# Kernel tuning notes

Measured on AMD Instinct MI355X. Metric: run time of the kernel, lower is better.

The kernel has to match this reference:

```python
import jax, jax.numpy as jnp
import numpy as np

B, S, IN_DIM = 4, 2048, 768
D, M, K, H = 24, 8192, 32, 256
Q = 8
SCALES = 4
TWO_PI = 2.0 * np.pi


def _ln(x, g, b):
    m = jnp.mean(x, -1, keepdims=True)
    v = jnp.mean((x - m) ** 2, -1, keepdims=True)
    return (x - m) * jax.lax.rsqrt(v + 1e-5) * g + b


def setup_inputs() -> dict:
    key = jax.random.key(0)
    ks = jax.random.split(key, 12)
    def n(k, shape, s=0.02):
        return (jax.random.normal(k, shape) * s).astype(jnp.float32)
    f32 = jnp.float32
    return dict(
        x=jax.random.normal(ks[0], (B, S, IN_DIM), dtype=f32),
        W_in=n(ks[1], (3 * D, IN_DIM)), b_in=jnp.zeros((3 * D,), f32),
        ln_in_g=jnp.ones((3 * D,), f32), ln_in_b=jnp.zeros((3 * D,), f32),
        ricci=jnp.eye(D, dtype=f32),
        fractal_w=jnp.ones((SCALES,), f32),
        keys=jax.random.normal(ks[2], (M, D), dtype=f32),
        key_phase_W=n(ks[3], (H, IN_DIM)), key_phase_b=jnp.zeros((H,), f32),
        entangle_key=n(ks[4], (H,), 0.1),
        holo_re=n(ks[5], (M, H), 0.1), holo_im=n(ks[6], (M, H), 0.1),
        readout_W=n(ks[7], (3 * D, 2 * H)), readout_b=jnp.zeros((3 * D,), f32),
        W_out=n(ks[8], (IN_DIM, 3 * D)), b_out=jnp.zeros((IN_DIM,), f32),
        ln_out_g=jnp.ones((IN_DIM,), f32), ln_out_b=jnp.zeros((IN_DIM,), f32),
        quantum_phase=jax.random.normal(ks[9], (M, Q), dtype=f32),
    )


def reference(x, W_in, b_in, ln_in_g, ln_in_b, ricci, fractal_w, keys,
              key_phase_W, key_phase_b, entangle_key, holo_re, holo_im,
              readout_W, readout_b, W_out, b_out, ln_out_g, ln_out_b,
              quantum_phase):
    # encode_to_manifold: Linear -> LN -> GELU -> view (B,S,D,3) -> ricci einsum
    z = jax.nn.gelu(_ln(x @ W_in.T + b_in, ln_in_g, ln_in_b), approximate=False)
    z = z.reshape(B, S, D, 3)
    z = jnp.einsum('bseq,ed->bsdq', z, ricci)
    q = z.mean(axis=3)  # (B,S,D)

    # fractal cdist: cdist(q/2^s, k/2^s) = cdist(q,k)/2^s -> single pass * factor
    d2 = (jnp.sum(q * q, -1)[..., None]
          + jnp.sum(keys * keys, -1)[None, None, :]
          - 2.0 * jnp.einsum('bsd,md->bsm', q, keys))
    d = jnp.sqrt(jnp.maximum(d2, 0.0))  # (B,S,M)
    fw = jax.nn.softmax(fractal_w)
    scale = jnp.sum(fw / (2.0 ** jnp.arange(SCALES, dtype=jnp.float32)))
    dist = d * scale  # temperature buffer == 1.0

    # top-K smallest distances
    neg_top, itop = jax.lax.top_k(-dist, K)  # (B,S,K)
    w = jax.nn.softmax(neg_top, axis=-1)     # softmax(-dtop)

    # holographic read: unbind with conj(key) from gathered holograms
    phase = TWO_PI * jax.nn.sigmoid(x @ key_phase_W.T + key_phase_b)  # (B,S,H)
    Kf = jnp.fft.fft(jnp.exp(1j * phase), axis=-1) * jnp.exp(1j * entangle_key)
    Hol = holo_re + 1j * holo_im  # (M,H) complex
    # weighted sum over slots first, then multiply conj(Kf) (same math, cheaper)
    Hmix = jnp.einsum('bsk,bskh->bsh', w.astype(Hol.dtype), Hol[itop])
    vhat = jnp.fft.ifft(jnp.conj(Kf) * Hmix, axis=-1)
    feat = jnp.concatenate([vhat.real, vhat.imag], axis=-1)  # (B,S,2H)

    triplet = feat @ readout_W.T + readout_b
    out = jax.nn.gelu(_ln(triplet @ W_out.T + b_out, ln_out_g, ln_out_b),
                      approximate=False)

    # quantum gain (any_fire = False for this configuration)
    phases = jnp.tanh(quantum_phase[itop]).mean(-1)  # (B,S,K)
    gain = 1.0 + 0.02 * jnp.sum(w * phases, -1, keepdims=True)
    return out * gain
```

## Files before the change

kernel.cpp:

```cpp
#include <hip/hip_runtime.h>
#include <hip/hip_bf16.h>
#include <math.h>

#define NROWS 8192
#define INDIM 768
#define TD    72
#define DM    24
#define MKEYS 8192
#define KSEL  32
#define HN    256
#define K3CAND 128

#define TWO_PI_F 6.283185307179586f

typedef __attribute__((ext_vector_type(8))) short short8_t;
typedef __attribute__((ext_vector_type(4))) float f32x4;

__device__ __forceinline__ float gelu_exact(float v){
  return 0.5f * v * (1.0f + erff(v * 0.7071067811865476f));
}

__device__ __forceinline__ unsigned short bf16rn(float f){
  unsigned u = __float_as_uint(f);
  unsigned r = u + 0x7FFFu + ((u >> 16) & 1u);
  return (unsigned short)(r >> 16);
}

__device__ __forceinline__ float rowmin16(float v){
  int s, p;
  s = __float_as_int(v); p = __builtin_amdgcn_update_dpp(s, s, 0x111, 0xF, 0xF, false);
  v = fminf(v, __int_as_float(p));
  s = __float_as_int(v); p = __builtin_amdgcn_update_dpp(s, s, 0x112, 0xF, 0xF, false);
  v = fminf(v, __int_as_float(p));
  s = __float_as_int(v); p = __builtin_amdgcn_update_dpp(s, s, 0x114, 0xF, 0xF, false);
  v = fminf(v, __int_as_float(p));
  s = __float_as_int(v); p = __builtin_amdgcn_update_dpp(s, s, 0x118, 0xF, 0xF, false);
  v = fminf(v, __int_as_float(p));
  return v;
}

__global__ __launch_bounds__(256) void k0_gprep(
    const float* __restrict__ RW, float* __restrict__ Grp, float* __restrict__ Gip)
{
  __shared__ float sre[16][260];
  __shared__ float sim_[16][260];
  __shared__ float twc[HN], tws[HN];
  const int t = threadIdx.x;
  const int o0 = blockIdx.x * 16;
  {
    const float a = (float)t * (TWO_PI_F / 256.f);
    twc[t] = cosf(a); tws[t] = sinf(a);
  }
  const int r = t >> 4, cg = t & 15;
  const int o = o0 + r;
#pragma unroll
  for (int j = 0; j < 16; j++) {
    const int n = cg + 16 * j;
    const int hb = __brev((unsigned)n) >> 24;
    float cr = 0.f, ci = 0.f;
    if (o < TD) { cr = RW[(size_t)o * 512 + n]; ci = RW[(size_t)o * 512 + 256 + n]; }
    sre[r][hb] = cr; sim_[r][hb] = ci;
  }
  __syncthreads();
  const int t16 = t & 15;
  for (int s = 0; s < 8; s++) {
    const int half = 1 << s;
#pragma unroll
    for (int p = 0; p < 8; p++) {
      const int bi = t16 + 16 * p;
      const int jj = bi & (half - 1);
      const int base = (bi >> s) << (s + 1);
      const int i0 = base + jj, i1 = i0 + half;
      const int tw = jj << (7 - s);
      const float wr = twc[tw], wi = -tws[tw];
      const float ar = sre[r][i0], ai = sim_[r][i0];
      const float br = sre[r][i1], b2 = sim_[r][i1];
      const float tr = wr * br - wi * b2, ti = wr * b2 + wi * br;
      sre[r][i0] = ar + tr; sim_[r][i0] = ai + ti;
      sre[r][i1] = ar - tr; sim_[r][i1] = ai - ti;
    }
    __syncthreads();
  }
#pragma unroll
  for (int p = 0; p < 16; p++) {
    const int h = t16 + 16 * p;
    const size_t base = ((size_t)(h >> 2) * 128 + o) * 4 + (h & 3);
    Grp[base] = sre[r][h];
    Gip[base] = sim_[r][h];
  }
}

__global__ __launch_bounds__(256) void kw_split(
    const float* __restrict__ Wp, unsigned short* __restrict__ Wphi,
    unsigned short* __restrict__ Wplo)
{
  const int i4 = blockIdx.x * 256 + threadIdx.x;
  const float4 v = ((const float4*)Wp)[i4];
  float vv[4] = {v.x, v.y, v.z, v.w};
  ushort4 hh, ll;
  unsigned short* hp = (unsigned short*)&hh;
  unsigned short* lp = (unsigned short*)&ll;
#pragma unroll
  for (int j = 0; j < 4; j++) {
    const unsigned short h = bf16rn(vv[j]);
    const float hf = __uint_as_float(((unsigned)h) << 16);
    hp[j] = h; lp[j] = bf16rn(vv[j] - hf);
  }
  ((ushort4*)Wphi)[i4] = hh;
  ((ushort4*)Wplo)[i4] = ll;
}

__global__ __launch_bounds__(256) void kwo_split(
    const float* __restrict__ Wo, unsigned short* __restrict__ Wohi,
    unsigned short* __restrict__ Wolo)
{
  const int idx = blockIdx.x * 256 + threadIdx.x;
  const int row = idx / 96, k = idx % 96;
  const float v = (k < TD) ? Wo[(size_t)row * TD + k] : 0.f;
  const unsigned short h = bf16rn(v);
  const float hf = __uint_as_float(((unsigned)h) << 16);
  Wohi[idx] = h;
  Wolo[idx] = bf16rn(v - hf);
}

__global__ __launch_bounds__(256) void k1_encode(
    const float* __restrict__ x, const float* __restrict__ Wi,
    const float* __restrict__ bi, const float* __restrict__ gi,
    const float* __restrict__ bbi, const float* __restrict__ ricci,
    float* __restrict__ qvec, float* __restrict__ qnorm)
{
  __shared__ float xs[16][132];
  __shared__ float Ws[TD][132];
  __shared__ float zs[16][73];
  __shared__ float zb[16][25];
  const int t = threadIdx.x;
  const int r2 = t >> 4, ks = (t >> 3) & 1, u = t & 7;
  const int row0 = blockIdx.x * 16;

  float acc[9];
#pragma unroll
  for (int j = 0; j < 9; j++) acc[j] = 0.f;

  for (int kc = 0; kc < 6; kc++) {
    __syncthreads();
#pragma unroll
    for (int i = 0; i < 2; i++) {
      int idx = t + 256 * i;
      int rr = idx >> 5, kk = (idx & 31) << 2;
      *(float4*)&xs[rr][kk] = *(const float4*)&x[(size_t)(row0 + rr) * INDIM + kc * 128 + kk];
    }
#pragma unroll
    for (int i = 0; i < 9; i++) {
      int idx = t + 256 * i;
      int rr = idx >> 5, kk = (idx & 31) << 2;
      *(float4*)&Ws[rr][kk] = *(const float4*)&Wi[(size_t)rr * INDIM + kc * 128 + kk];
    }
    __syncthreads();
    const int kb = ks * 64;
#pragma unroll 4
    for (int kq = 0; kq < 16; kq++) {
      const float4 xv = *(const float4*)&xs[r2][kb + kq * 4];
#pragma unroll
      for (int j = 0; j < 9; j++) {
        const float4 wv = *(const float4*)&Ws[u + 8 * j][kb + kq * 4];
        acc[j] = fmaf(xv.x, wv.x, fmaf(xv.y, wv.y, fmaf(xv.z, wv.z, fmaf(xv.w, wv.w, acc[j]))));
      }
    }
  }
#pragma unroll
  for (int j = 0; j < 9; j++) acc[j] += __shfl_xor(acc[j], 8);

  float yv[9];
  float ps = 0.f, pq = 0.f;
#pragma unroll
  for (int j = 0; j < 9; j++) {
    const int o = u + 8 * j;
    yv[j] = acc[j] + bi[o];
    ps += yv[j]; pq += yv[j] * yv[j];
  }
#pragma unroll
  for (int m = 1; m < 8; m <<= 1) { ps += __shfl_xor(ps, m); pq += __shfl_xor(pq, m); }
  const float mean = ps * (1.f / 72.f);
  const float var  = pq * (1.f / 72.f) - mean * mean;
  const float rstd = rsqrtf(var + 1e-5f);
#pragma unroll
  for (int j = 0; j < 9; j++) {
    const int o = u + 8 * j;
    const float z = gelu_exact((yv[j] - mean) * rstd * gi[o] + bbi[o]);
    if (ks == 0) zs[r2][o] = z;
  }
  __syncthreads();
  {
    const int kt = t & 15;
    for (int e = kt; e < 24; e += 16)
      zb[r2][e] = (zs[r2][3 * e] + zs[r2][3 * e + 1] + zs[r2][3 * e + 2]) * (1.f / 3.f);
  }
  __syncthreads();
  {
    const int kt = t & 15;
    float qnp = 0.f;
    for (int d = kt; d < 24; d += 16) {
      float qd = 0.f;
#pragma unroll
      for (int e = 0; e < 24; e++) qd = fmaf(zb[r2][e], ricci[e * 24 + d], qd);
      qvec[(size_t)(row0 + r2) * DM + d] = qd;
      qnp = fmaf(qd, qd, qnp);
    }
#pragma unroll
    for (int m = 1; m < 16; m <<= 1) qnp += __shfl_xor(qnp, m, 16);
    if (kt == 0) qnorm[row0 + r2] = qnp;
  }
}

__global__ __launch_bounds__(256) void k2_prep(
    const float* __restrict__ keys, const float* __restrict__ qp,
    float* __restrict__ kn, float* __restrict__ pm,
    unsigned short* __restrict__ khi, unsigned short* __restrict__ klo,
    float* __restrict__ kmx)
{
  __shared__ float red[256];
  const int t = threadIdx.x;
  const int m = blockIdx.x * 256 + t;
  float kv[24];
#pragma unroll
  for (int d = 0; d < DM; d += 4) {
    const float4 v = *(const float4*)&keys[(size_t)m * DM + d];
    kv[d] = v.x; kv[d + 1] = v.y; kv[d + 2] = v.z; kv[d + 3] = v.w;
  }
  float s = 0.f;
#pragma unroll
  for (int d = 0; d < DM; d++) s = fmaf(kv[d], kv[d], s);
  kn[m] = s;
  float p = 0.f;
#pragma unroll
  for (int q = 0; q < 8; q++) p += tanhf(qp[(size_t)m * 8 + q]);
  pm[m] = p * 0.125f;
#pragma unroll
  for (int d = 0; d < DM; d++) {
    const unsigned short h = bf16rn(kv[d]);
    const float hf = __uint_as_float(((unsigned)h) << 16);
    const unsigned short l = bf16rn(kv[d] - hf);
    khi[(size_t)m * 32 + d] = h;
    klo[(size_t)m * 32 + d] = l;
  }
#pragma unroll
  for (int d = DM; d < 32; d++) { khi[(size_t)m * 32 + d] = 0; klo[(size_t)m * 32 + d] = 0; }
  red[t] = s;
  __syncthreads();
  for (int off = 128; off > 0; off >>= 1) {
    if (t < off) red[t] = fmaxf(red[t], red[t + off]);
    __syncthreads();
  }
  if (t == 0) kmx[blockIdx.x] = red[0];
}

__global__ __launch_bounds__(1024, 4) void k3_topk(
    const float* __restrict__ qvec, const float* __restrict__ qnorm,
    const float* __restrict__ keys, const float* __restrict__ kn,
    const unsigned short* __restrict__ khi, const unsigned short* __restrict__ klo,
    const float* __restrict__ kmx,
    const float* __restrict__ fw,  const float* __restrict__ pm,
    float* __restrict__ w_out, int* __restrict__ itop_out, float* __restrict__ gain_out)
{
  __shared__ float qsm[32][25];
  __shared__ float qns[32];
  __shared__ unsigned short qh_l[32][32];
  __shared__ unsigned short ql_l[32][32];
  __shared__ float gmins[64][33];
  __shared__ float Ts[32];
  __shared__ float Tm2s[32];
  __shared__ unsigned glive[2];
  __shared__ int cnt[32];
  __shared__ int      candI[32][K3CAND];
  __shared__ unsigned candV[32][K3CAND];
  __shared__ float wV[32][KSEL];
  __shared__ int   wI[32][KSEL];
  __shared__ float knmax_s;

  const int t = threadIdx.x;
  const int w = t >> 6, lane = t & 63;
  const int colid = lane & 15;
  const int kgrp  = lane >> 4;
  const int row0 = blockIdx.x * 32;

  if (t < 32 * DM) qsm[t / DM][t % DM] = qvec[(size_t)row0 * DM + t];
  if (t < 32) { qns[t] = qnorm[row0 + t]; cnt[t] = 0; }
  if (t < 2) glive[t] = 0u;
  if (t == 0) { float m = 0.f; for (int i = 0; i < 32; i++) m = fmaxf(m, kmx[i]); knmax_s = m; }
  __syncthreads();
  {
    const int r = t >> 5, k = t & 31;
    const float v = (k < DM) ? qsm[r][k] : 0.f;
    const unsigned short h = bf16rn(v);
    const float hf = __uint_as_float(((unsigned)h) << 16);
    qh_l[r][k] = h;
    ql_l[r][k] = bf16rn(v - hf);
  }
  __syncthreads();

  const short8_t ah0 = *(const short8_t*)&qh_l[colid][kgrp * 8];
  const short8_t al0 = *(const short8_t*)&ql_l[colid][kgrp * 8];
  const short8_t ah1 = *(const short8_t*)&qh_l[16 + colid][kgrp * 8];
  const short8_t al1 = *(const short8_t*)&ql_l[16 + colid][kgrp * 8];
  float qn8[8];
#pragma unroll
  for (int reg = 0; reg < 4; reg++) {
    qn8[reg]     = qns[kgrp * 4 + reg];
    qn8[reg + 4] = qns[16 + kgrp * 4 + reg];
  }

  for (int u = 0; u < 4; u++) {
    const int g = w + 16 * u;
    const int nbase = g * 128;
    float mn[8];
#pragma unroll
    for (int j = 0; j < 8; j++) {
      const int key = nbase + j * 16 + colid;
      const short8_t bh = *(const short8_t*)&khi[(size_t)key * 32 + kgrp * 8];
      const short8_t bl = *(const short8_t*)&klo[(size_t)key * 32 + kgrp * 8];
      const float knv = kn[key];
      f32x4 c0 = {0.f, 0.f, 0.f, 0.f}, c1 = {0.f, 0.f, 0.f, 0.f};
      c0 = __builtin_amdgcn_mfma_f32_16x16x32_bf16(ah0, bh, c0, 0, 0, 0);
      c1 = __builtin_amdgcn_mfma_f32_16x16x32_bf16(ah1, bh, c1, 0, 0, 0);
      c0 = __builtin_amdgcn_mfma_f32_16x16x32_bf16(ah0, bl, c0, 0, 0, 0);
      c1 = __builtin_amdgcn_mfma_f32_16x16x32_bf16(ah1, bl, c1, 0, 0, 0);
      c0 = __builtin_amdgcn_mfma_f32_16x16x32_bf16(al0, bh, c0, 0, 0, 0);
      c1 = __builtin_amdgcn_mfma_f32_16x16x32_bf16(al1, bh, c1, 0, 0, 0);
#pragma unroll
      for (int reg = 0; reg < 4; reg++) {
        const float d0 = fmaf(-2.f, c0[reg], qn8[reg] + knv);
        const float d1 = fmaf(-2.f, c1[reg], qn8[reg + 4] + knv);
        if (j == 0) { mn[reg] = d0; mn[reg + 4] = d1; }
        else        { mn[reg] = fminf(mn[reg], d0); mn[reg + 4] = fminf(mn[reg + 4], d1); }
      }
    }
#pragma unroll
    for (int reg = 0; reg < 4; reg++) {
      const float v0 = rowmin16(mn[reg]);
      const float v1 = rowmin16(mn[reg + 4]);
      if (colid == 15) {
        gmins[g][kgrp * 4 + reg] = v0;
        gmins[g][16 + kgrp * 4 + reg] = v1;
      }
    }
  }
  __syncthreads();

  {
    const int r = t & 31, i = t >> 5;
    const float v0 = gmins[i * 2][r], v1 = gmins[i * 2 + 1][r];
    int rk0 = 0, eq0 = 0, rk1 = 0, eq1 = 0;
    for (int g = 0; g < 64; g++) {
      const float gv = gmins[g][r];
      rk0 += (gv < v0); eq0 += (gv == v0);
      rk1 += (gv < v1); eq1 += (gv == v1);
    }
    if (rk0 <= 31 && rk0 + eq0 > 31) Ts[r] = v0;
    if (rk1 <= 31 && rk1 + eq1 > 31) Ts[r] = v1;
  }
  __syncthreads();
  if (t < 32) {
    const float T = Ts[t];
    const float mu = 2e-4f * sqrtf(fmaxf(qns[t], 0.f) * knmax_s) + 1e-6f;
    Tm2s[t] = T + fabsf(T) * 1e-6f + 2.f * mu;
  }
  __syncthreads();
  {
    const int r = t & 31, i = t >> 5;
    const unsigned b0 = (gmins[i * 2][r]     <= Tm2s[r]) ? 1u : 0u;
    const unsigned b1 = (gmins[i * 2 + 1][r] <= Tm2s[r]) ? 2u : 0u;
    const unsigned bits = (b0 | b1) << ((i * 2) & 31);
    if (bits) atomicOr(&glive[i >> 4], bits);
  }
  __syncthreads();

  float tm8[8];
#pragma unroll
  for (int reg = 0; reg < 4; reg++) {
    tm8[reg]     = Tm2s[kgrp * 4 + reg];
    tm8[reg + 4] = Tm2s[16 + kgrp * 4 + reg];
  }

  for (int u = 0; u < 4; u++) {
    const int g = w + 16 * u;
    if (!((glive[g >> 5] >> (g & 31)) & 1u)) continue;
    const int nbase = g * 128;
#pragma unroll
    for (int j = 0; j < 8; j++) {
      const int key = nbase + j * 16 + colid;
      const short8_t bh = *(const short8_t*)&khi[(size_t)key * 32 + kgrp * 8];
      const short8_t bl = *(const short8_t*)&klo[(size_t)key * 32 + kgrp * 8];
      const float knv = kn[key];
      f32x4 c0 = {0.f, 0.f, 0.f, 0.f}, c1 = {0.f, 0.f, 0.f, 0.f};
      c0 = __builtin_amdgcn_mfma_f32_16x16x32_bf16(ah0, bh, c0, 0, 0, 0);
      c1 = __builtin_amdgcn_mfma_f32_16x16x32_bf16(ah1, bh, c1, 0, 0, 0);
      c0 = __builtin_amdgcn_mfma_f32_16x16x32_bf16(ah0, bl, c0, 0, 0, 0);
      c1 = __builtin_amdgcn_mfma_f32_16x16x32_bf16(ah1, bl, c1, 0, 0, 0);
      c0 = __builtin_amdgcn_mfma_f32_16x16x32_bf16(al0, bh, c0, 0, 0, 0);
      c1 = __builtin_amdgcn_mfma_f32_16x16x32_bf16(al1, bh, c1, 0, 0, 0);
#pragma unroll
      for (int reg = 0; reg < 4; reg++) {
        const float d0 = fmaf(-2.f, c0[reg], qn8[reg] + knv);
        if (d0 <= tm8[reg]) {
          const int row = kgrp * 4 + reg;
          const int pos = atomicAdd(&cnt[row], 1);
          if (pos < K3CAND) candI[row][pos] = key;
        }
        const float d1 = fmaf(-2.f, c1[reg], qn8[reg + 4] + knv);
        if (d1 <= tm8[reg + 4]) {
          const int row = 16 + kgrp * 4 + reg;
          const int pos = atomicAdd(&cnt[row], 1);
          if (pos < K3CAND) candI[row][pos] = key;
        }
      }
    }
  }
  for (int idx = t; idx < 32 * KSEL; idx += 1024) { wV[idx >> 5][idx & 31] = 1e30f; wI[idx >> 5][idx & 31] = 0; }
  __syncthreads();

  {
    const int r = t >> 5, kt = t & 31;
    const int C = min(cnt[r], K3CAND);
    const float qnr = qns[r];
    for (int ci = kt; ci < C; ci += 32) {
      const int key = candI[r][ci];
      float kv[24];
#pragma unroll
      for (int d = 0; d < DM; d += 4) {
        const float4 v = *(const float4*)&keys[(size_t)key * DM + d];
        kv[d] = v.x; kv[d + 1] = v.y; kv[d + 2] = v.z; kv[d + 3] = v.w;
      }
      float dot = 0.f;
#pragma unroll
      for (int d = 0; d < DM; d++) dot = fmaf(kv[d], qsm[r][d], dot);
      const float d2 = fmaf(-2.f, dot, qnr + kn[key]);
      candV[r][ci] = __float_as_uint(fmaxf(d2, 0.f));
    }
  }
  __syncthreads();

  {
    const int r = t >> 5, kt = t & 31;
    const int C = min(cnt[r], K3CAND);
    for (int ci = kt; ci < C; ci += 32) {
      const unsigned v = candV[r][ci];
      const unsigned key = (unsigned)candI[r][ci];
      int rk = 0;
      for (int j = 0; j < C; j++) {
        const unsigned vj = candV[r][j];
        rk += (vj < v) || (vj == v && (unsigned)candI[r][j] < key);
      }
      if (rk < KSEL) { wV[r][rk] = __uint_as_float(v); wI[r][rk] = (int)key; }
    }
  }
  __syncthreads();

  float sc;
  {
    const float f0 = fw[0], f1 = fw[1], f2 = fw[2], f3 = fw[3];
    const float mx = fmaxf(fmaxf(f0, f1), fmaxf(f2, f3));
    const float e0 = expf(f0 - mx), e1 = expf(f1 - mx), e2 = expf(f2 - mx), e3 = expf(f3 - mx);
    sc = (e0 + 0.5f * e1 + 0.25f * e2 + 0.125f * e3) / (e0 + e1 + e2 + e3);
  }
  if (t < 512) {
    const int r = t >> 4, kt = t & 15;
    const float dA = sqrtf(wV[r][kt]) * sc;
    const float dB = sqrtf(wV[r][kt + 16]) * sc;
    float mn = fminf(dA, dB);
#pragma unroll
    for (int m = 1; m < 16; m <<= 1) mn = fminf(mn, __shfl_xor(mn, m, 16));
    const float eA = expf(mn - dA), eB = expf(mn - dB);
    float s = eA + eB;
#pragma unroll
    for (int m = 1; m < 16; m <<= 1) s += __shfl_xor(s, m, 16);
    const float w0 = eA / s, w1 = eB / s;
    const int k0 = wI[r][kt], k1 = wI[r][kt + 16];
    float gp = w0 * pm[k0] + w1 * pm[k1];
#pragma unroll
    for (int m = 1; m < 16; m <<= 1) gp += __shfl_xor(gp, m, 16);
    const size_t row = (size_t)(row0 + r);
    w_out[row * KSEL + kt] = w0;      w_out[row * KSEL + kt + 16] = w1;
    itop_out[row * KSEL + kt] = k0;   itop_out[row * KSEL + kt + 16] = k1;
    if (kt == 0) gain_out[row] = 1.f + 0.02f * gp;
  }
}

__global__ __launch_bounds__(512) void k4a_pgemm(
    const float* __restrict__ x, const unsigned short* __restrict__ Wphi,
    const unsigned short* __restrict__ Wplo, const float* __restrict__ bp,
    float* __restrict__ p)
{
  const int t = threadIdx.x;
  const int w = t >> 6, lane = t & 63;
  const int colid = lane & 15, kgrp = lane >> 4;
  const int wm = w >> 2, wn = w & 3;
  const int row0 = blockIdx.x * 32;
  const int arow = row0 + wm * 16 + colid;

  f32x4 acc0 = {0.f, 0.f, 0.f, 0.f};
  f32x4 acc1 = {0.f, 0.f, 0.f, 0.f};
  f32x4 acc2 = {0.f, 0.f, 0.f, 0.f};
  f32x4 acc3 = {0.f, 0.f, 0.f, 0.f};

  for (int kc = 0; kc < 24; kc++) {
    const int kb = kc * 32 + kgrp * 8;
    float xv[8];
    *(float4*)&xv[0] = *(const float4*)&x[(size_t)arow * INDIM + kb];
    *(float4*)&xv[4] = *(const float4*)&x[(size_t)arow * INDIM + kb + 4];
    short8_t ah, al;
#pragma unroll
    for (int i = 0; i < 8; i++) {
      const unsigned short h = bf16rn(xv[i]);
      const float hf = __uint_as_float(((unsigned)h) << 16);
      ah[i] = (short)h;
      al[i] = (short)bf16rn(xv[i] - hf);
    }
#pragma unroll
    for (int ct = 0; ct < 4; ct++) {
      const int col = wn * 64 + ct * 16 + colid;
      const short8_t bh = *(const short8_t*)&Wphi[(size_t)col * INDIM + kb];
      const short8_t bl = *(const short8_t*)&Wplo[(size_t)col * INDIM + kb];
      f32x4* pa = (ct == 0) ? &acc0 : (ct == 1) ? &acc1 : (ct == 2) ? &acc2 : &acc3;
      *pa = __builtin_amdgcn_mfma_f32_16x16x32_bf16(ah, bh, *pa, 0, 0, 0);
      *pa = __builtin_amdgcn_mfma_f32_16x16x32_bf16(al, bh, *pa, 0, 0, 0);
      *pa = __builtin_amdgcn_mfma_f32_16x16x32_bf16(ah, bl, *pa, 0, 0, 0);
    }
  }
#pragma unroll
  for (int ct = 0; ct < 4; ct++) {
    const int col = wn * 64 + ct * 16 + colid;
    const float b = bp[col];
    const f32x4 a = (ct == 0) ? acc0 : (ct == 1) ? acc1 : (ct == 2) ? acc2 : acc3;
#pragma unroll
    for (int reg = 0; reg < 4; reg++) {
      const int row = row0 + wm * 16 + kgrp * 4 + reg;
      p[(size_t)row * HN + col] = a[reg] + b;
    }
  }
}

__global__ __launch_bounds__(256) void k4b_fft(
    const float* __restrict__ p, const float* __restrict__ ek,
    float* __restrict__ kf_re, float* __restrict__ kf_im)
{
  __shared__ float2 c[16][273];
  __shared__ float twc[HN], tws[HN];
  const int t = threadIdx.x;
  const int row0 = blockIdx.x * 16;
  {
    const float a = (float)t * (TWO_PI_F / 256.f);
    twc[t] = cosf(a); tws[t] = sinf(a);
  }
  {
    const int hb = __brev((unsigned)t) >> 24;
    const int hbi = hb + (hb >> 5);
#pragma unroll
    for (int i = 0; i < 16; i++) {
      const float pv = p[(size_t)(row0 + i) * HN + t];
      const float sg = 1.f / (1.f + expf(-pv));
      float sn, cs;
      __sincosf(TWO_PI_F * sg, &sn, &cs);
      c[i][hbi] = make_float2(cs, sn);
    }
  }
  __syncthreads();
  const int r = t >> 4, t16 = t & 15;
  for (int s = 0; s < 8; s++) {
    const int half = 1 << s;
#pragma unroll
    for (int pp = 0; pp < 8; pp++) {
      const int bi = t16 + 16 * pp;
      const int jj = bi & (half - 1);
      const int base = (bi >> s) << (s + 1);
      const int i0 = base + jj, i1 = i0 + half;
      const int tw = jj << (7 - s);
      const float wr = twc[tw], wi = -tws[tw];
      const int p0 = i0 + (i0 >> 5), p1 = i1 + (i1 >> 5);
      const float2 A = c[r][p0];
      const float2 B = c[r][p1];
      const float tr = wr * B.x - wi * B.y, ti = wr * B.y + wi * B.x;
      c[r][p0] = make_float2(A.x + tr, A.y + ti);
      c[r][p1] = make_float2(A.x - tr, A.y - ti);
    }
    __syncthreads();
  }
  {
    float esn, ecs;
    __sincosf(ek[t], &esn, &ecs);
    const int ti = t + (t >> 5);
#pragma unroll
    for (int i = 0; i < 16; i++) {
      const float2 v = c[i][ti];
      const size_t o = (size_t)(row0 + i) * HN + t;
      kf_re[o] = v.x * ecs - v.y * esn;
      kf_im[o] = v.x * esn + v.y * ecs;
    }
  }
}

__global__ __launch_bounds__(256) void k5_holo(
    const float* __restrict__ holo_re, const float* __restrict__ holo_im,
    const float* __restrict__ kf_re, const float* __restrict__ kf_im,
    const float* __restrict__ w_ws, const int* __restrict__ itop_ws,
    const float* __restrict__ Grp, const float* __restrict__ Gip,
    const float* __restrict__ rb, float* __restrict__ triplet)
{
  __shared__ __align__(16) float ysr[8][260];
  __shared__ __align__(16) float ysi[8][260];
  __shared__ float red[4][8][128];
  __shared__ float wsm[8][KSEL];
  __shared__ int   ism[8][KSEL];
  const int t = threadIdx.x;
  const int w = t >> 6, lane = t & 63;
  const int row0 = blockIdx.x * 8;

  {
    const int rr = t >> 5, k2 = t & 31;
    wsm[rr][k2] = w_ws[(size_t)(row0 + rr) * KSEL + k2];
    ism[rr][k2] = itop_ws[(size_t)(row0 + rr) * KSEL + k2];
  }
  __syncthreads();

#pragma unroll
  for (int pass = 0; pass < 2; pass++) {
    const int row = w + 4 * pass;
    float4 hr4 = {0.f, 0.f, 0.f, 0.f};
    float4 hi4 = {0.f, 0.f, 0.f, 0.f};
#pragma unroll 8
    for (int k2 = 0; k2 < KSEL; k2++) {
      const int m = ism[row][k2];
      const float wk = wsm[row][k2];
      const float4 re4 = *(const float4*)&holo_re[(size_t)m * HN + lane * 4];
      const float4 im4 = *(const float4*)&holo_im[(size_t)m * HN + lane * 4];
      hr4.x = fmaf(wk, re4.x, hr4.x); hr4.y = fmaf(wk, re4.y, hr4.y);
      hr4.z = fmaf(wk, re4.z, hr4.z); hr4.w = fmaf(wk, re4.w, hr4.w);
      hi4.x = fmaf(wk, im4.x, hi4.x); hi4.y = fmaf(wk, im4.y, hi4.y);
      hi4.z = fmaf(wk, im4.z, hi4.z); hi4.w = fmaf(wk, im4.w, hi4.w);
    }
    const size_t o = (size_t)(row0 + row) * HN + lane * 4;
    const float4 kr4 = *(const float4*)&kf_re[o];
    const float4 ki4 = *(const float4*)&kf_im[o];
    float4 yr4, yi4;
    yr4.x = kr4.x * hr4.x + ki4.x * hi4.x;  yi4.x = kr4.x * hi4.x - ki4.x * hr4.x;
    yr4.y = kr4.y * hr4.y + ki4.y * hi4.y;  yi4.y = kr4.y * hi4.y - ki4.y * hr4.y;
    yr4.z = kr4.z * hr4.z + ki4.z * hi4.z;  yi4.z = kr4.z * hi4.z - ki4.z * hr4.z;
    yr4.w = kr4.w * hr4.w + ki4.w * hi4.w;  yi4.w = kr4.w * hi4.w - ki4.w * hr4.w;
    *(float4*)&ysr[row][lane * 4] = yr4;
    *(float4*)&ysi[row][lane * 4] = yi4;
  }
  __syncthreads();

  float acc[8][2];
#pragma unroll
  for (int rr = 0; rr < 8; rr++) { acc[rr][0] = 0.f; acc[rr][1] = 0.f; }
#pragma unroll 4
  for (int i = 0; i < 16; i++) {
    const int h4 = w * 16 + i;
    const float4 gra = *(const float4*)&Grp[((size_t)h4 * 128 + lane) * 4];
    const float4 gia = *(const float4*)&Gip[((size_t)h4 * 128 + lane) * 4];
    const float4 grb = *(const float4*)&Grp[((size_t)h4 * 128 + 64 + lane) * 4];
    const float4 gib = *(const float4*)&Gip[((size_t)h4 * 128 + 64 + lane) * 4];
#pragma unroll
    for (int rr = 0; rr < 8; rr++) {
      const float4 yr4 = *(const float4*)&ysr[rr][h4 * 4];
      const float4 yi4 = *(const float4*)&ysi[rr][h4 * 4];
      acc[rr][0] = fmaf(yr4.x, gra.x, fmaf(yr4.y, gra.y, fmaf(yr4.z, gra.z, fmaf(yr4.w, gra.w, acc[rr][0]))));
      acc[rr][0] = fmaf(yi4.x, gia.x, fmaf(yi4.y, gia.y, fmaf(yi4.z, gia.z, fmaf(yi4.w, gia.w, acc[rr][0]))));
      acc[rr][1] = fmaf(yr4.x, grb.x, fmaf(yr4.y, grb.y, fmaf(yr4.z, grb.z, fmaf(yr4.w, grb.w, acc[rr][1]))));
      acc[rr][1] = fmaf(yi4.x, gib.x, fmaf(yi4.y, gib.y, fmaf(yi4.z, gib.z, fmaf(yi4.w, gib.w, acc[rr][1]))));
    }
  }
#pragma unroll
  for (int rr = 0; rr < 8; rr++) {
    red[w][rr][lane] = acc[rr][0];
    red[w][rr][64 + lane] = acc[rr][1];
  }
  __syncthreads();

  for (int idx = t; idx < 8 * 128; idx += 256) {
    const int rr = idx >> 7, o = idx & 127;
    if (o < TD) {
      const float s = red[0][rr][o] + red[1][rr][o] + red[2][rr][o] + red[3][rr][o];
      triplet[(size_t)(row0 + rr) * TD + o] = rb[o] + s * (1.f / 256.f);
    }
  }
}

__global__ __launch_bounds__(256) void k6_mfma(
    const float* __restrict__ triplet, const unsigned short* __restrict__ Wohi,
    const unsigned short* __restrict__ Wolo, const float* __restrict__ bo,
    const float* __restrict__ go, const float* __restrict__ bbo,
    const float* __restrict__ gain, float* __restrict__ out)
{
  __shared__ float ys[16][772];
  const int t = threadIdx.x;
  const int w = t >> 6, lane = t & 63;
  const int colid = lane & 15, kgrp = lane >> 4;
  const int row0 = blockIdx.x * 16;
  const int arow = row0 + colid;

  f32x4 acc[12];
#pragma unroll
  for (int ct = 0; ct < 12; ct++) acc[ct] = (f32x4){0.f, 0.f, 0.f, 0.f};

#pragma unroll
  for (int kc = 0; kc < 3; kc++) {
    const int kb = kc * 32 + kgrp * 8;
    float xv[8];
    if (kb < TD) {
      *(float4*)&xv[0] = *(const float4*)&triplet[(size_t)arow * TD + kb];
      *(float4*)&xv[4] = *(const float4*)&triplet[(size_t)arow * TD + kb + 4];
    } else {
#pragma unroll
      for (int i = 0; i < 8; i++) xv[i] = 0.f;
    }
    short8_t ah, al;
#pragma unroll
    for (int i = 0; i < 8; i++) {
      const unsigned short h = bf16rn(xv[i]);
      const float hf = __uint_as_float(((unsigned)h) << 16);
      ah[i] = (short)h; al[i] = (short)bf16rn(xv[i] - hf);
    }
#pragma unroll
    for (int ct = 0; ct < 12; ct++) {
      const int col = w * 192 + ct * 16 + colid;
      const short8_t bh = *(const short8_t*)&Wohi[(size_t)col * 96 + kb];
      const short8_t bl = *(const short8_t*)&Wolo[(size_t)col * 96 + kb];
      acc[ct] = __builtin_amdgcn_mfma_f32_16x16x32_bf16(ah, bh, acc[ct], 0, 0, 0);
      acc[ct] = __builtin_amdgcn_mfma_f32_16x16x32_bf16(al, bh, acc[ct], 0, 0, 0);
      acc[ct] = __builtin_amdgcn_mfma_f32_16x16x32_bf16(ah, bl, acc[ct], 0, 0, 0);
    }
  }
#pragma unroll
  for (int ct = 0; ct < 12; ct++) {
    const int col = w * 192 + ct * 16 + colid;
    const float b = bo[col];
#pragma unroll
    for (int reg = 0; reg < 4; reg++)
      ys[kgrp * 4 + reg][col] = acc[ct][reg] + b;
  }
  __syncthreads();

  const int r = t >> 4, kt = t & 15;
  float s = 0.f, sq = 0.f;
  for (int u = 0; u < 48; u++) {
    const float v = ys[r][kt + 16 * u];
    s += v; sq = fmaf(v, v, sq);
  }
#pragma unroll
  for (int m = 1; m < 16; m <<= 1) { s += __shfl_xor(s, m, 16); sq += __shfl_xor(sq, m, 16); }
  const float mean = s * (1.f / 768.f);
  const float var  = sq * (1.f / 768.f) - mean * mean;
  const float rstd = rsqrtf(var + 1e-5f);
  const float gn = gain[row0 + r];
  for (int u = 0; u < 48; u++) {
    const int e = kt + 16 * u;
    const float v = (ys[r][e] - mean) * rstd * go[e] + bbo[e];
    out[(size_t)(row0 + r) * INDIM + e] = gelu_exact(v) * gn;
  }
}

extern "C" void kernel_launch(void* const* d_in, const int* in_sizes, int n_in,
                              void* d_out, int out_size, void* d_ws, size_t ws_size,
                              hipStream_t stream)
{
  (void)in_sizes; (void)n_in; (void)out_size; (void)ws_size;
  const float* x     = (const float*)d_in[0];
  const float* Wi    = (const float*)d_in[1];
  const float* bi    = (const float*)d_in[2];
  const float* gi    = (const float*)d_in[3];
  const float* bbi   = (const float*)d_in[4];
  const float* ricci = (const float*)d_in[5];
  const float* fw    = (const float*)d_in[6];
  const float* keys  = (const float*)d_in[7];
  const float* Wp    = (const float*)d_in[8];
  const float* bp    = (const float*)d_in[9];
  const float* ek    = (const float*)d_in[10];
  const float* hre   = (const float*)d_in[11];
  const float* him   = (const float*)d_in[12];
  const float* RW    = (const float*)d_in[13];
  const float* rb    = (const float*)d_in[14];
  const float* Wo    = (const float*)d_in[15];
  const float* bo    = (const float*)d_in[16];
  const float* go    = (const float*)d_in[17];
  const float* bbo   = (const float*)d_in[18];
  const float* qp    = (const float*)d_in[19];
  float* out = (float*)d_out;

  char* ws = (char*)d_ws;
  float* qvec    = (float*)(ws + 0);
  float* qnorm   = (float*)(ws + 786432);
  float* kn      = (float*)(ws + 819200);
  float* pm      = (float*)(ws + 851968);
  float* gain    = (float*)(ws + 884736);
  float* w_ws    = (float*)(ws + 917504);
  int*   itop    = (int*)  (ws + 1966080);
  float* triplet = (float*)(ws + 3014656);
  float* kf_re   = (float*)(ws + 5373952);
  float* kf_im   = (float*)(ws + 13762560);
  unsigned short* khi = (unsigned short*)(ws + 22151168);
  unsigned short* klo = (unsigned short*)(ws + 22675456);
  float* kmx     = (float*)(ws + 23199744);
  float* Grp     = (float*)(ws + 23200768);
  float* Gip     = (float*)(ws + 23331840);
  unsigned short* Wphi = (unsigned short*)(ws + 23462912);
  unsigned short* Wplo = (unsigned short*)(ws + 23856128);
  float* pbuf    = (float*)(ws + 24249344);
  unsigned short* Wohi = (unsigned short*)(ws + 32637952);
  unsigned short* Wolo = (unsigned short*)(ws + 32785408);

  k0_gprep<<<dim3(8), dim3(256), 0, stream>>>(RW, Grp, Gip);
  kw_split<<<dim3(192), dim3(256), 0, stream>>>(Wp, Wphi, Wplo);
  kwo_split<<<dim3(288), dim3(256), 0, stream>>>(Wo, Wohi, Wolo);
  k2_prep<<<dim3(MKEYS / 256), dim3(256), 0, stream>>>(keys, qp, kn, pm, khi, klo, kmx);
  k1_encode<<<dim3(NROWS / 16), dim3(256), 0, stream>>>(x, Wi, bi, gi, bbi, ricci, qvec, qnorm);
  k4a_pgemm<<<dim3(NROWS / 32), dim3(512), 0, stream>>>(x, Wphi, Wplo, bp, pbuf);
  k4b_fft<<<dim3(NROWS / 16), dim3(256), 0, stream>>>(pbuf, ek, kf_re, kf_im);
  k3_topk<<<dim3(NROWS / 32), dim3(1024), 0, stream>>>(qvec, qnorm, keys, kn, khi, klo, kmx, fw, pm, w_ws, itop, gain);
  k5_holo<<<dim3(NROWS / 8), dim3(256), 0, stream>>>(hre, him, kf_re, kf_im, w_ws, itop, Grp, Gip, rb, triplet);
  k6_mfma<<<dim3(NROWS / 16), dim3(256), 0, stream>>>(triplet, Wohi, Wolo, bo, go, bbo, gain, out);
}
```

Before: 267.7 us.

## Halve rows per top-k block to 16 and double grid size

Result: slower. 302.2 us (+12.9%).

```diff
diff --git a/kernel.cpp b/kernel.cpp
--- a/kernel.cpp
+++ b/kernel.cpp
@@ -254,7 +254,7 @@
   if (t == 0) kmx[blockIdx.x] = red[0];
 }
 
-__global__ __launch_bounds__(1024, 4) void k3_topk(
+__global__ __launch_bounds__(1024, 8) void k3_topk(
     const float* __restrict__ qvec, const float* __restrict__ qnorm,
     const float* __restrict__ keys, const float* __restrict__ kn,
     const unsigned short* __restrict__ khi, const unsigned short* __restrict__ klo,
@@ -262,33 +262,33 @@
     const float* __restrict__ fw,  const float* __restrict__ pm,
     float* __restrict__ w_out, int* __restrict__ itop_out, float* __restrict__ gain_out)
 {
-  __shared__ float qsm[32][25];
-  __shared__ float qns[32];
-  __shared__ unsigned short qh_l[32][32];
-  __shared__ unsigned short ql_l[32][32];
-  __shared__ float gmins[64][33];
-  __shared__ float Ts[32];
-  __shared__ float Tm2s[32];
+  __shared__ float qsm[16][25];
+  __shared__ float qns[16];
+  __shared__ unsigned short qh_l[16][32];
+  __shared__ unsigned short ql_l[16][32];
+  __shared__ float gmins[64][17];
+  __shared__ float Ts[16];
+  __shared__ float Tm2s[16];
   __shared__ unsigned glive[2];
-  __shared__ int cnt[32];
-  __shared__ int      candI[32][K3CAND];
-  __shared__ unsigned candV[32][K3CAND];
-  __shared__ float wV[32][KSEL];
-  __shared__ int   wI[32][KSEL];
+  __shared__ int cnt[16];
+  __shared__ int      candI[16][K3CAND];
+  __shared__ unsigned candV[16][K3CAND];
+  __shared__ float wV[16][KSEL];
+  __shared__ int   wI[16][KSEL];
   __shared__ float knmax_s;
 
   const int t = threadIdx.x;
   const int w = t >> 6, lane = t & 63;
   const int colid = lane & 15;
   const int kgrp  = lane >> 4;
-  const int row0 = blockIdx.x * 32;
-
-  if (t < 32 * DM) qsm[t / DM][t % DM] = qvec[(size_t)row0 * DM + t];
-  if (t < 32) { qns[t] = qnorm[row0 + t]; cnt[t] = 0; }
+  const int row0 = blockIdx.x * 16;
+
+  if (t < 16 * DM) qsm[t / DM][t % DM] = qvec[(size_t)row0 * DM + t];
+  if (t < 16) { qns[t] = qnorm[row0 + t]; cnt[t] = 0; }
   if (t < 2) glive[t] = 0u;
   if (t == 0) { float m = 0.f; for (int i = 0; i < 32; i++) m = fmaxf(m, kmx[i]); knmax_s = m; }
   __syncthreads();
-  {
+  if (t < 512) {
     const int r = t >> 5, k = t & 31;
     const float v = (k < DM) ? qsm[r][k] : 0.f;
     const unsigned short h = bf16rn(v);
@@ -300,86 +300,65 @@
 
   const short8_t ah0 = *(const short8_t*)&qh_l[colid][kgrp * 8];
   const short8_t al0 = *(const short8_t*)&ql_l[colid][kgrp * 8];
-  const short8_t ah1 = *(const short8_t*)&qh_l[16 + colid][kgrp * 8];
-  const short8_t al1 = *(const short8_t*)&ql_l[16 + colid][kgrp * 8];
-  float qn8[8];
-#pragma unroll
-  for (int reg = 0; reg < 4; reg++) {
-    qn8[reg]     = qns[kgrp * 4 + reg];
-    qn8[reg + 4] = qns[16 + kgrp * 4 + reg];
-  }
+  float qn4[4];
+#pragma unroll
+  for (int reg = 0; reg < 4; reg++) qn4[reg] = qns[kgrp * 4 + reg];
 
   for (int u = 0; u < 4; u++) {
     const int g = w + 16 * u;
     const int nbase = g * 128;
-    float mn[8];
+    float mn[4];
 #pragma unroll
     for (int j = 0; j < 8; j++) {
       const int key = nbase + j * 16 + colid;
       const short8_t bh = *(const short8_t*)&khi[(size_t)key * 32 + kgrp * 8];
       const short8_t bl = *(const short8_t*)&klo[(size_t)key * 32 + kgrp * 8];
       const float knv = kn[key];
-      f32x4 c0 = {0.f, 0.f, 0.f, 0.f}, c1 = {0.f, 0.f, 0.f, 0.f};
+      f32x4 c0 = {0.f, 0.f, 0.f, 0.f};
       c0 = __builtin_amdgcn_mfma_f32_16x16x32_bf16(ah0, bh, c0, 0, 0, 0);
-      c1 = __builtin_amdgcn_mfma_f32_16x16x32_bf16(ah1, bh, c1, 0, 0, 0);
       c0 = __builtin_amdgcn_mfma_f32_16x16x32_bf16(ah0, bl, c0, 0, 0, 0);
-      c1 = __builtin_amdgcn_mfma_f32_16x16x32_bf16(ah1, bl, c1, 0, 0, 0);
       c0 = __builtin_amdgcn_mfma_f32_16x16x32_bf16(al0, bh, c0, 0, 0, 0);
-      c1 = __builtin_amdgcn_mfma_f32_16x16x32_bf16(al1, bh, c1, 0, 0, 0);
 #pragma unroll
       for (int reg = 0; reg < 4; reg++) {
-        const float d0 = fmaf(-2.f, c0[reg], qn8[reg] + knv);
-        const float d1 = fmaf(-2.f, c1[reg], qn8[reg + 4] + knv);
-        if (j == 0) { mn[reg] = d0; mn[reg + 4] = d1; }
-        else        { mn[reg] = fminf(mn[reg], d0); mn[reg + 4] = fminf(mn[reg + 4], d1); }
+        const float d0 = fmaf(-2.f, c0[reg], qn4[reg] + knv);
+        if (j == 0) mn[reg] = d0;
+        else        mn[reg] = fminf(mn[reg], d0);
       }
     }
 #pragma unroll
     for (int reg = 0; reg < 4; reg++) {
       const float v0 = rowmin16(mn[reg]);
-      const float v1 = rowmin16(mn[reg + 4]);
-      if (colid == 15) {
-        gmins[g][kgrp * 4 + reg] = v0;
-        gmins[g][16 + kgrp * 4 + reg] = v1;
-      }
-    }
-  }
-  __syncthreads();
-
-  {
-    const int r = t & 31, i = t >> 5;
-    const float v0 = gmins[i * 2][r], v1 = gmins[i * 2 + 1][r];
-    int rk0 = 0, eq0 = 0, rk1 = 0, eq1 = 0;
+      if (colid == 15) gmins[g][kgrp * 4 + reg] = v0;
+    }
+  }
+  __syncthreads();
+
+  {
+    const int r = t & 15, i = t >> 4;
+    const float v0 = gmins[i][r];
+    int rk0 = 0, eq0 = 0;
     for (int g = 0; g < 64; g++) {
       const float gv = gmins[g][r];
       rk0 += (gv < v0); eq0 += (gv == v0);
-      rk1 += (gv < v1); eq1 += (gv == v1);
     }
     if (rk0 <= 31 && rk0 + eq0 > 31) Ts[r] = v0;
-    if (rk1 <= 31 && rk1 + eq1 > 31) Ts[r] = v1;
-  }
-  __syncthreads();
-  if (t < 32) {
+  }
+  __syncthreads();
+  if (t < 16) {
     const float T = Ts[t];
     const float mu = 2e-4f * sqrtf(fmaxf(qns[t], 0.f) * knmax_s) + 1e-6f;
     Tm2s[t] = T + fabsf(T) * 1e-6f + 2.f * mu;
   }
   __syncthreads();
   {
-    const int r = t & 31, i = t >> 5;
-    const unsigned b0 = (gmins[i * 2][r]     <= Tm2s[r]) ? 1u : 0u;
-    const unsigned b1 = (gmins[i * 2 + 1][r] <= Tm2s[r]) ? 2u : 0u;
-    const unsigned bits = (b0 | b1) << ((i * 2) & 31);
-    if (bits) atomicOr(&glive[i >> 4], bits);
-  }
-  __syncthreads();
-
-  float tm8[8];
-#pragma unroll
-  for (int reg = 0; reg < 4; reg++) {
-    tm8[reg]     = Tm2s[kgrp * 4 + reg];
-    tm8[reg + 4] = Tm2s[16 + kgrp * 4 + reg];
-  }
+    const int r = t & 15, i = t >> 4;
+    if (gmins[i][r] <= Tm2s[r]) atomicOr(&glive[i >> 5], 1u << (i & 31));
+  }
+  __syncthreads();
+
+  float tm4[4];
+#pragma unroll
+  for (int reg = 0; reg < 4; reg++) tm4[reg] = Tm2s[kgrp * 4 + reg];
 
   for (int u = 0; u < 4; u++) {
     const int g = w + 16 * u;
@@ -391,38 +370,29 @@
       const short8_t bh = *(const short8_t*)&khi[(size_t)key * 32 + kgrp * 8];
       const short8_t bl = *(const short8_t*)&klo[(size_t)key * 32 + kgrp * 8];
       const float knv = kn[key];
-      f32x4 c0 = {0.f, 0.f, 0.f, 0.f}, c1 = {0.f, 0.f, 0.f, 0.f};
+      f32x4 c0 = {0.f, 0.f, 0.f, 0.f};
       c0 = __builtin_amdgcn_mfma_f32_16x16x32_bf16(ah0, bh, c0, 0, 0, 0);
-      c1 = __builtin_amdgcn_mfma_f32_16x16x32_bf16(ah1, bh, c1, 0, 0, 0);
       c0 = __builtin_amdgcn_mfma_f32_16x16x32_bf16(ah0, bl, c0, 0, 0, 0);
-      c1 = __builtin_amdgcn_mfma_f32_16x16x32_bf16(ah1, bl, c1, 0, 0, 0);
       c0 = __builtin_amdgcn_mfma_f32_16x16x32_bf16(al0, bh, c0, 0, 0, 0);
-      c1 = __builtin_amdgcn_mfma_f32_16x16x32_bf16(al1, bh, c1, 0, 0, 0);
 #pragma unroll
       for (int reg = 0; reg < 4; reg++) {
-        const float d0 = fmaf(-2.f, c0[reg], qn8[reg] + knv);
-        if (d0 <= tm8[reg]) {
+        const float d0 = fmaf(-2.f, c0[reg], qn4[reg] + knv);
+        if (d0 <= tm4[reg]) {
           const int row = kgrp * 4 + reg;
           const int pos = atomicAdd(&cnt[row], 1);
           if (pos < K3CAND) candI[row][pos] = key;
         }
-        const float d1 = fmaf(-2.f, c1[reg], qn8[reg + 4] + knv);
-        if (d1 <= tm8[reg + 4]) {
-          const int row = 16 + kgrp * 4 + reg;
-          const int pos = atomicAdd(&cnt[row], 1);
-          if (pos < K3CAND) candI[row][pos] = key;
-        }
       }
     }
   }
-  for (int idx = t; idx < 32 * KSEL; idx += 1024) { wV[idx >> 5][idx & 31] = 1e30f; wI[idx >> 5][idx & 31] = 0; }
-  __syncthreads();
-
-  {
-    const int r = t >> 5, kt = t & 31;
+  for (int idx = t; idx < 16 * KSEL; idx += 1024) { wV[idx >> 5][idx & 31] = 1e30f; wI[idx >> 5][idx & 31] = 0; }
+  __syncthreads();
+
+  {
+    const int r = t >> 6, kt = t & 63;
     const int C = min(cnt[r], K3CAND);
     const float qnr = qns[r];
-    for (int ci = kt; ci < C; ci += 32) {
+    for (int ci = kt; ci < C; ci += 64) {
       const int key = candI[r][ci];
       float kv[24];
 #pragma unroll
@@ -440,9 +410,9 @@
   __syncthreads();
 
   {
-    const int r = t >> 5, kt = t & 31;
+    const int r = t >> 6, kt = t & 63;
     const int C = min(cnt[r], K3CAND);
-    for (int ci = kt; ci < C; ci += 32) {
+    for (int ci = kt; ci < C; ci += 64) {
       const unsigned v = candV[r][ci];
       const unsigned key = (unsigned)candI[r][ci];
       int rk = 0;
@@ -462,7 +432,7 @@
     const float e0 = expf(f0 - mx), e1 = expf(f1 - mx), e2 = expf(f2 - mx), e3 = expf(f3 - mx);
     sc = (e0 + 0.5f * e1 + 0.25f * e2 + 0.125f * e3) / (e0 + e1 + e2 + e3);
   }
-  if (t < 512) {
+  if (t < 256) {
     const int r = t >> 4, kt = t & 15;
     const float dA = sqrtf(wV[r][kt]) * sc;
     const float dB = sqrtf(wV[r][kt + 16]) * sc;
@@ -816,7 +786,7 @@
   k1_encode<<<dim3(NROWS / 16), dim3(256), 0, stream>>>(x, Wi, bi, gi, bbi, ricci, qvec, qnorm);
   k4a_pgemm<<<dim3(NROWS / 32), dim3(512), 0, stream>>>(x, Wphi, Wplo, bp, pbuf);
   k4b_fft<<<dim3(NROWS / 16), dim3(256), 0, stream>>>(pbuf, ek, kf_re, kf_im);
-  k3_topk<<<dim3(NROWS / 32), dim3(1024), 0, stream>>>(qvec, qnorm, keys, kn, khi, klo, kmx, fw, pm, w_ws, itop, gain);
+  k3_topk<<<dim3(NROWS / 16), dim3(1024), 0, stream>>>(qvec, qnorm, keys, kn, khi, klo, kmx, fw, pm, w_ws, itop, gain);
   k5_holo<<<dim3(NROWS / 8), dim3(256), 0, stream>>>(hre, him, kf_re, kf_im, w_ws, itop, Grp, Gip, rb, triplet);
   k6_mfma<<<dim3(NROWS / 16), dim3(256), 0, stream>>>(triplet, Wohi, Wolo, bo, go, bbo, gain, out);
 }
```

## Split top-k kernel into three stages with key-halves parallelism

Applied to the files above, without the earlier changes.

New measurement: 318.0 us. +18.8%, slower.

```diff
diff --git a/kernel.cpp b/kernel.cpp
--- a/kernel.cpp
+++ b/kernel.cpp
@@ -254,39 +254,26 @@
   if (t == 0) kmx[blockIdx.x] = red[0];
 }
 
-__global__ __launch_bounds__(1024, 4) void k3_topk(
+__global__ __launch_bounds__(1024, 4) void k3a_gmins(
     const float* __restrict__ qvec, const float* __restrict__ qnorm,
-    const float* __restrict__ keys, const float* __restrict__ kn,
     const unsigned short* __restrict__ khi, const unsigned short* __restrict__ klo,
-    const float* __restrict__ kmx,
-    const float* __restrict__ fw,  const float* __restrict__ pm,
-    float* __restrict__ w_out, int* __restrict__ itop_out, float* __restrict__ gain_out)
+    const float* __restrict__ kn, float* __restrict__ gmg)
 {
   __shared__ float qsm[32][25];
   __shared__ float qns[32];
   __shared__ unsigned short qh_l[32][32];
   __shared__ unsigned short ql_l[32][32];
-  __shared__ float gmins[64][33];
-  __shared__ float Ts[32];
-  __shared__ float Tm2s[32];
-  __shared__ unsigned glive[2];
-  __shared__ int cnt[32];
-  __shared__ int      candI[32][K3CAND];
-  __shared__ unsigned candV[32][K3CAND];
-  __shared__ float wV[32][KSEL];
-  __shared__ int   wI[32][KSEL];
-  __shared__ float knmax_s;
+  __shared__ float gml[32][33];
 
   const int t = threadIdx.x;
   const int w = t >> 6, lane = t & 63;
-  const int colid = lane & 15;
-  const int kgrp  = lane >> 4;
-  const int row0 = blockIdx.x * 32;
+  const int colid = lane & 15, kgrp = lane >> 4;
+  const int bx = blockIdx.x;
+  const int rc = bx >> 1, half = bx & 1;
+  const int row0 = rc * 32;
 
   if (t < 32 * DM) qsm[t / DM][t % DM] = qvec[(size_t)row0 * DM + t];
-  if (t < 32) { qns[t] = qnorm[row0 + t]; cnt[t] = 0; }
-  if (t < 2) glive[t] = 0u;
-  if (t == 0) { float m = 0.f; for (int i = 0; i < 32; i++) m = fmaxf(m, kmx[i]); knmax_s = m; }
+  if (t < 32) qns[t] = qnorm[row0 + t];
   __syncthreads();
   {
     const int r = t >> 5, k = t & 31;
@@ -309,9 +296,9 @@
     qn8[reg + 4] = qns[16 + kgrp * 4 + reg];
   }
 
-  for (int u = 0; u < 4; u++) {
-    const int g = w + 16 * u;
-    const int nbase = g * 128;
+  for (int u = 0; u < 2; u++) {
+    const int gl = w + 16 * u;
+    const int nbase = (half * 32 + gl) * 128;
     float mn[8];
 #pragma unroll
     for (int j = 0; j < 8; j++) {
@@ -339,12 +326,70 @@
       const float v0 = rowmin16(mn[reg]);
       const float v1 = rowmin16(mn[reg + 4]);
       if (colid == 15) {
-        gmins[g][kgrp * 4 + reg] = v0;
-        gmins[g][16 + kgrp * 4 + reg] = v1;
+        gml[gl][kgrp * 4 + reg] = v0;
+        gml[gl][16 + kgrp * 4 + reg] = v1;
       }
     }
   }
   __syncthreads();
+  {
+    const int gl = t >> 5, r = t & 31;
+    gmg[(size_t)(half * 32 + gl) * NROWS + row0 + r] = gml[gl][r];
+  }
+}
+
+__global__ __launch_bounds__(1024, 4) void k3b_passB(
+    const float* __restrict__ qvec, const float* __restrict__ qnorm,
+    const unsigned short* __restrict__ khi, const unsigned short* __restrict__ klo,
+    const float* __restrict__ kn, const float* __restrict__ kmx,
+    const float* __restrict__ gmg, int* __restrict__ cntg, int* __restrict__ candIg)
+{
+  __shared__ float qsm[32][25];
+  __shared__ float qns[32];
+  __shared__ unsigned short qh_l[32][32];
+  __shared__ unsigned short ql_l[32][32];
+  __shared__ float gmins[64][33];
+  __shared__ float Ts[32];
+  __shared__ float Tm2s[32];
+  __shared__ unsigned glive[2];
+  __shared__ float knmax_s;
+
+  const int t = threadIdx.x;
+  const int w = t >> 6, lane = t & 63;
+  const int colid = lane & 15, kgrp = lane >> 4;
+  const int bx = blockIdx.x;
+  const int rc = bx >> 1, half = bx & 1;
+  const int row0 = rc * 32;
+
+  if (t < 32 * DM) qsm[t / DM][t % DM] = qvec[(size_t)row0 * DM + t];
+  if (t < 32) qns[t] = qnorm[row0 + t];
+  if (t < 2) glive[t] = 0u;
+  if (t == 0) { float m = 0.f; for (int i = 0; i < 32; i++) m = fmaxf(m, kmx[i]); knmax_s = m; }
+  for (int idx = t; idx < 64 * 32; idx += 1024) {
+    const int g = idx >> 5, r = idx & 31;
+    gmins[g][r] = gmg[(size_t)g * NROWS + row0 + r];
+  }
+  __syncthreads();
+  {
+    const int r = t >> 5, k = t & 31;
+    const float v = (k < DM) ? qsm[r][k] : 0.f;
+    const unsigned short h = bf16rn(v);
+    const float hf = __uint_as_float(((unsigned)h) << 16);
+    qh_l[r][k] = h;
+    ql_l[r][k] = bf16rn(v - hf);
+  }
+  __syncthreads();
+
+  const short8_t ah0 = *(const short8_t*)&qh_l[colid][kgrp * 8];
+  const short8_t al0 = *(const short8_t*)&ql_l[colid][kgrp * 8];
+  const short8_t ah1 = *(const short8_t*)&qh_l[16 + colid][kgrp * 8];
+  const short8_t al1 = *(const short8_t*)&ql_l[16 + colid][kgrp * 8];
+  float qn8[8];
+#pragma unroll
+  for (int reg = 0; reg < 4; reg++) {
+    qn8[reg]     = qns[kgrp * 4 + reg];
+    qn8[reg + 4] = qns[16 + kgrp * 4 + reg];
+  }
 
   {
     const int r = t & 31, i = t >> 5;
@@ -381,8 +426,8 @@
     tm8[reg + 4] = Tm2s[16 + kgrp * 4 + reg];
   }
 
-  for (int u = 0; u < 4; u++) {
-    const int g = w + 16 * u;
+  for (int u = 0; u < 2; u++) {
+    const int g = half * 32 + (w + 16 * u);
     if (!((glive[g >> 5] >> (g & 31)) & 1u)) continue;
     const int nbase = g * 128;
 #pragma unroll
@@ -402,27 +447,54 @@
       for (int reg = 0; reg < 4; reg++) {
         const float d0 = fmaf(-2.f, c0[reg], qn8[reg] + knv);
         if (d0 <= tm8[reg]) {
-          const int row = kgrp * 4 + reg;
-          const int pos = atomicAdd(&cnt[row], 1);
-          if (pos < K3CAND) candI[row][pos] = key;
+          const int row = row0 + kgrp * 4 + reg;
+          const int pos = atomicAdd(&cntg[row], 1);
+          if (pos < K3CAND) candIg[(size_t)row * K3CAND + pos] = key;
         }
         const float d1 = fmaf(-2.f, c1[reg], qn8[reg + 4] + knv);
         if (d1 <= tm8[reg + 4]) {
-          const int row = 16 + kgrp * 4 + reg;
-          const int pos = atomicAdd(&cnt[row], 1);
-          if (pos < K3CAND) candI[row][pos] = key;
+          const int row = row0 + 16 + kgrp * 4 + reg;
+          const int pos = atomicAdd(&cntg[row], 1);
+          if (pos < K3CAND) candIg[(size_t)row * K3CAND + pos] = key;
         }
       }
     }
   }
-  for (int idx = t; idx < 32 * KSEL; idx += 1024) { wV[idx >> 5][idx & 31] = 1e30f; wI[idx >> 5][idx & 31] = 0; }
-  __syncthreads();
-
-  {
-    const int r = t >> 5, kt = t & 31;
-    const int C = min(cnt[r], K3CAND);
+}
+
+__global__ __launch_bounds__(512) void k3c_select(
+    const float* __restrict__ qvec, const float* __restrict__ qnorm,
+    const float* __restrict__ keys, const float* __restrict__ kn,
+    const float* __restrict__ fw, const float* __restrict__ pm,
+    const int* __restrict__ cntg, const int* __restrict__ candIg,
+    float* __restrict__ w_out, int* __restrict__ itop_out, float* __restrict__ gain_out)
+{
+  __shared__ float qsm[32][25];
+  __shared__ float qns[32];
+  __shared__ int cnts[32];
+  __shared__ int      candI[32][K3CAND];
+  __shared__ unsigned candV[32][K3CAND];
+  __shared__ float wV[32][KSEL];
+  __shared__ int   wI[32][KSEL];
+
+  const int t = threadIdx.x;
+  const int row0 = blockIdx.x * 32;
+
+  for (int idx = t; idx < 32 * DM; idx += 512) qsm[idx / DM][idx % DM] = qvec[(size_t)row0 * DM + idx];
+  if (t < 32) { qns[t] = qnorm[row0 + t]; cnts[t] = min(cntg[row0 + t], K3CAND); }
+  __syncthreads();
+  for (int idx = t; idx < 32 * K3CAND; idx += 512) {
+    const int r = idx >> 7, c2 = idx & (K3CAND - 1);
+    if (c2 < cnts[r]) candI[r][c2] = candIg[(size_t)(row0 + r) * K3CAND + c2];
+  }
+  for (int idx = t; idx < 32 * KSEL; idx += 512) { wV[idx >> 5][idx & 31] = 1e30f; wI[idx >> 5][idx & 31] = 0; }
+  __syncthreads();
+
+  {
+    const int r = t >> 4, kt = t & 15;
+    const int C = cnts[r];
     const float qnr = qns[r];
-    for (int ci = kt; ci < C; ci += 32) {
+    for (int ci = kt; ci < C; ci += 16) {
       const int key = candI[r][ci];
       float kv[24];
 #pragma unroll
@@ -440,9 +512,9 @@
   __syncthreads();
 
   {
-    const int r = t >> 5, kt = t & 31;
-    const int C = min(cnt[r], K3CAND);
-    for (int ci = kt; ci < C; ci += 32) {
+    const int r = t >> 4, kt = t & 15;
+    const int C = cnts[r];
+    for (int ci = kt; ci < C; ci += 16) {
       const unsigned v = candV[r][ci];
       const unsigned key = (unsigned)candI[r][ci];
       int rk = 0;
@@ -462,7 +534,7 @@
     const float e0 = expf(f0 - mx), e1 = expf(f1 - mx), e2 = expf(f2 - mx), e3 = expf(f3 - mx);
     sc = (e0 + 0.5f * e1 + 0.25f * e2 + 0.125f * e3) / (e0 + e1 + e2 + e3);
   }
-  if (t < 512) {
+  {
     const int r = t >> 4, kt = t & 15;
     const float dA = sqrtf(wV[r][kt]) * sc;
     const float dB = sqrtf(wV[r][kt + 16]) * sc;
@@ -808,6 +880,9 @@
   float* pbuf    = (float*)(ws + 24249344);
   unsigned short* Wohi = (unsigned short*)(ws + 32637952);
   unsigned short* Wolo = (unsigned short*)(ws + 32785408);
+  float* gmg     = (float*)(ws + 24249344);
+  int*   cntg    = (int*)  (ws + 26346496);
+  int*   candIg  = (int*)  (ws + 26379264);
 
   k0_gprep<<<dim3(8), dim3(256), 0, stream>>>(RW, Grp, Gip);
   kw_split<<<dim3(192), dim3(256), 0, stream>>>(Wp, Wphi, Wplo);
@@ -816,7 +891,10 @@
   k1_encode<<<dim3(NROWS / 16), dim3(256), 0, stream>>>(x, Wi, bi, gi, bbi, ricci, qvec, qnorm);
   k4a_pgemm<<<dim3(NROWS / 32), dim3(512), 0, stream>>>(x, Wphi, Wplo, bp, pbuf);
   k4b_fft<<<dim3(NROWS / 16), dim3(256), 0, stream>>>(pbuf, ek, kf_re, kf_im);
-  k3_topk<<<dim3(NROWS / 32), dim3(1024), 0, stream>>>(qvec, qnorm, keys, kn, khi, klo, kmx, fw, pm, w_ws, itop, gain);
+  hipMemsetAsync(cntg, 0, NROWS * sizeof(int), stream);
+  k3a_gmins<<<dim3(512), dim3(1024), 0, stream>>>(qvec, qnorm, khi, klo, kn, gmg);
+  k3b_passB<<<dim3(512), dim3(1024), 0, stream>>>(qvec, qnorm, khi, klo, kn, kmx, gmg, cntg, candIg);
+  k3c_select<<<dim3(256), dim3(512), 0, stream>>>(qvec, qnorm, keys, kn, fw, pm, cntg, candIg, w_ws, itop, gain);
   k5_holo<<<dim3(NROWS / 8), dim3(256), 0, stream>>>(hre, him, kf_re, kf_im, w_ws, itop, Grp, Gip, rb, triplet);
   k6_mfma<<<dim3(NROWS / 16), dim3(256), 0, stream>>>(triplet, Wohi, Wolo, bo, go, bbo, gain, out);
 }
```
